# Kernel optimization log

Hardware: AMD Instinct MI355X
Metric: run time of the kernel (lower is better)

The kernel has to match this reference:

```python
import jax, jax.numpy as jnp
import numpy as np

B, N, C, H = 2, 2048, 1024, 16
D = C // H  # head_dim = 64


def setup_inputs() -> dict:
    key = jax.random.key(0)
    ks = jax.random.split(key, 5)
    s = 0.02
    return {
        "x": jax.random.normal(ks[0], (B, N, C), dtype=jnp.float32),
        "w_qkv": jax.random.normal(ks[1], (3 * C, C), dtype=jnp.float32) * s,
        "b_qkv": jnp.zeros((3 * C,), dtype=jnp.float32),
        "w_proj": jax.random.normal(ks[2], (C, C), dtype=jnp.float32) * s,
        "b_proj": jnp.zeros((C,), dtype=jnp.float32),
    }


def reference(x, w_qkv, b_qkv, w_proj, b_proj):
    scale = D ** -0.5
    # QKV projection: [B,N,3C]
    qkv = jnp.einsum('bnc,oc->bno', x, w_qkv) + b_qkv
    qkv = qkv.reshape(B, N, 3, H, D).transpose(2, 0, 3, 1, 4)  # [3,B,H,N,D]
    q, k, v = qkv[0], qkv[1], qkv[2]
    attn = jnp.einsum('bhnd,bhmd->bhnm', q, k) * scale  # [B,H,N,N]
    attn = jax.nn.softmax(attn, axis=-1)
    out = jnp.einsum('bhnm,bhmd->bhnd', attn, v)  # [B,H,N,D]
    out = out.transpose(0, 2, 1, 3).reshape(B, N, C)
    return jnp.einsum('bnc,oc->bno', out, w_proj) + b_proj
```

## Files before the change

### kernel.cpp

```cpp
#include <hip/hip_runtime.h>
#include <hip/hip_bf16.h>

typedef __attribute__((ext_vector_type(4))) float f32x4;
typedef __attribute__((ext_vector_type(16))) float f32x16;
typedef __attribute__((ext_vector_type(8))) short short8;
typedef __attribute__((ext_vector_type(4))) unsigned int u32x4;
typedef __attribute__((ext_vector_type(2))) unsigned int u32x2;
typedef unsigned short u16;

__device__ __forceinline__ u16 f2bf(float x) {
  unsigned u = __float_as_uint(x);
  u += 0x7fffu + ((u >> 16) & 1u);
  return (u16)(u >> 16);
}

__device__ __forceinline__ void gload_lds16(const void* g, void* l) {
  __builtin_amdgcn_global_load_lds(
      (__attribute__((address_space(1))) void*)g,
      (__attribute__((address_space(3))) void*)l, 16, 0, 0);
}

__global__ void cvt_all(const float* __restrict__ x, const float* __restrict__ wq,
                        const float* __restrict__ wp, ushort4* __restrict__ dst) {
  const int N1 = 1048576, N2 = 786432, NT = 2097152;
  for (int i = blockIdx.x * 256 + threadIdx.x; i < NT; i += 524288) {
    float4 v;
    if (i < N1)            v = ((const float4*)x)[i];
    else if (i < N1 + N2)  v = ((const float4*)wq)[i - N1];
    else                   v = ((const float4*)wp)[i - N1 - N2];
    ushort4 o;
    o.x = f2bf(v.x); o.y = f2bf(v.y); o.z = f2bf(v.z); o.w = f2bf(v.w);
    dst[i] = o;
  }
}

__global__ __launch_bounds__(512, 2) void gemm256_bt(
    const u16* __restrict__ A, const u16* __restrict__ B,
    const float* __restrict__ bias, u16* __restrict__ Cout,
    int M, int N, int K)
{
  __shared__ u16 LA[2][2][8192];
  __shared__ u16 LB[2][12288];

  const int tid  = threadIdx.x;
  const int w    = tid >> 6;
  const int lane = tid & 63;
  const int wm   = w >> 2;
  const int wn   = w & 3;
  const int hi   = lane >> 4;
  const int lo   = lane & 15;

  const int L  = (int)(blockIdx.x & 7) * 32 + (int)(blockIdx.x >> 3);
  const int bx = L >> 4, by = L & 15;
  const long brow = (long)by * 256;
  const long bcol = (long)bx * 192;

  f32x4 acc[8][3];
#pragma unroll
  for (int m = 0; m < 8; ++m)
#pragma unroll
    for (int n = 0; n < 3; ++n)
#pragma unroll
      for (int r = 0; r < 4; ++r) acc[m][n][r] = 0.0f;

  const int srow = lane >> 3;
  const int sg   = (lane & 7) ^ srow;
  const int l7   = lo & 7;

  auto stA = [&](int kt, int bi, int i) {
    const long k0 = (long)kt * 64;
#pragma unroll
    for (int mh = 0; mh < 2; ++mh) {
      const long r = brow + mh * 128 + i * 64 + w * 8 + srow;
      gload_lds16(A + r * K + k0 + sg * 8, &LA[bi][mh][i * 4096 + w * 512]);
    }
  };
  auto stB = [&](int kt, int bi, int u) {
    const long k0 = (long)kt * 64;
    const long r = bcol + u * 64 + w * 8 + srow;
    gload_lds16(B + r * K + k0 + sg * 8, &LB[bi][u * 4096 + w * 512]);
  };

  short8 a[4][2], b[3][2];
  auto rdA = [&](int bi, int mq) {
#pragma unroll
    for (int f = 0; f < 4; ++f) {
      const int rl = mq * 64 + f * 16 + lo;
#pragma unroll
      for (int ks = 0; ks < 2; ++ks)
        a[f][ks] = *(const short8*)(&LA[bi][wm][rl * 64 + ((ks * 4 + hi) ^ l7) * 8]);
    }
  };
  auto rdB = [&](int bi) {
#pragma unroll
    for (int f = 0; f < 3; ++f) {
      const int rl = wn * 48 + f * 16 + lo;
#pragma unroll
      for (int ks = 0; ks < 2; ++ks)
        b[f][ks] = *(const short8*)(&LB[bi][rl * 64 + ((ks * 4 + hi) ^ l7) * 8]);
    }
  };

#define MFMA24(mq)                                                                  \
  __builtin_amdgcn_s_setprio(1);                                                    \
  _Pragma("unroll")                                                                 \
  for (int f = 0; f < 4; ++f)                                                       \
    _Pragma("unroll")                                                               \
    for (int n = 0; n < 3; ++n)                                                     \
      _Pragma("unroll")                                                             \
      for (int ks = 0; ks < 2; ++ks)                                                \
        acc[(mq)*4 + f][n] = __builtin_amdgcn_mfma_f32_16x16x32_bf16(               \
            a[f][ks], b[n][ks], acc[(mq)*4 + f][n], 0, 0, 0);                       \
  __builtin_amdgcn_s_setprio(0);

#define PHASE_WAIT()                                      \
  __builtin_amdgcn_s_barrier();                           \
  asm volatile("s_waitcnt lgkmcnt(0)" ::: "memory");      \
  __builtin_amdgcn_sched_barrier(0);

  const int nkt = K >> 6;
  stA(0, 0, 0); stA(0, 0, 1); stB(0, 0, 0); stB(0, 0, 1); stB(0, 0, 2);
  stA(1, 1, 0); stA(1, 1, 1); stB(1, 1, 0); stB(1, 1, 1); stB(1, 1, 2);
  asm volatile("s_waitcnt vmcnt(7)" ::: "memory");
  __builtin_amdgcn_s_barrier();

  for (int it = 0; it < (nkt >> 1); ++it) {
    const int t2 = 2 * it + 2, t3 = 2 * it + 3;
    rdA(0, 0); rdB(0);
    if (it > 0) stA(2 * it + 1, 1, 1);
    PHASE_WAIT(); MFMA24(0); __builtin_amdgcn_s_barrier();
    rdA(0, 1);
    if (t2 < nkt) { stB(t2, 0, 0); stB(t2, 0, 1); stB(t2, 0, 2); stA(t2, 0, 0); }
    PHASE_WAIT(); MFMA24(1);
    if (t2 < nkt) { asm volatile("s_waitcnt vmcnt(5)" ::: "memory"); }
    else          { asm volatile("s_waitcnt vmcnt(0)" ::: "memory"); }
    __builtin_amdgcn_sched_barrier(0);
    __builtin_amdgcn_s_barrier();
    rdA(1, 0); rdB(1);
    if (t2 < nkt) stA(t2, 0, 1);
    PHASE_WAIT(); MFMA24(0); __builtin_amdgcn_s_barrier();
    rdA(1, 1);
    if (t3 < nkt) { stB(t3, 1, 0); stB(t3, 1, 1); stB(t3, 1, 2); stA(t3, 1, 0); }
    PHASE_WAIT(); MFMA24(1);
    if (t3 < nkt) { asm volatile("s_waitcnt vmcnt(5)" ::: "memory"); }
    __builtin_amdgcn_sched_barrier(0);
    __builtin_amdgcn_s_barrier();
  }
#undef MFMA24
#undef PHASE_WAIT

  const float SCC = 0.18033688011112042f;
  float bv[3];
#pragma unroll
  for (int n = 0; n < 3; ++n) bv[n] = bias[bcol + wn * 48 + n * 16 + lo];
#pragma unroll
  for (int m = 0; m < 8; ++m)
#pragma unroll
    for (int n = 0; n < 3; ++n) {
      const long colf = bcol + wn * 48 + n * 16;
      const float qsc = (colf < 1024) ? SCC : 1.0f;
#pragma unroll
      for (int r = 0; r < 4; ++r) {
        const long row = brow + wm * 128 + m * 16 + hi * 4 + r;
        Cout[row * (long)N + colf + lo] = f2bf((acc[m][n][r] + bv[n]) * qsc);
      }
    }
}

template<int OUT_BF16>
__global__ __launch_bounds__(256) void gemm_bt(
    const u16* __restrict__ A, const u16* __restrict__ B,
    const float* __restrict__ bias, void* __restrict__ Cout,
    int M, int N, int K)
{
  __shared__ u16 As[2][128 * 64];
  __shared__ u16 Bs[2][128 * 64];
  const int tid  = threadIdx.x;
  const int lane = tid & 63;
  const int w    = tid >> 6;
  const int wm   = w >> 1, wn = w & 1;
  const int hi   = lane >> 4;
  const int lo   = lane & 15;
  const int l7   = lo & 7;
  const long brow = (long)blockIdx.y * 128;
  const long bcol = (long)blockIdx.x * 128;

  f32x4 acc[4][4];
#pragma unroll
  for (int i = 0; i < 4; i++)
#pragma unroll
    for (int j = 0; j < 4; j++)
#pragma unroll
      for (int r = 0; r < 4; r++) acc[i][j][r] = 0.0f;

  const int srow = lane >> 3;
  const int sg   = (lane & 7) ^ srow;

  float bv[4];
#pragma unroll
  for (int fn = 0; fn < 4; fn++) bv[fn] = bias[bcol + wn * 64 + fn * 16 + lo];

  auto stage = [&](int kt, int bi) {
    const int k0 = kt << 6;
#pragma unroll
    for (int c = 0; c < 4; ++c) {
      const int chunk = (c << 2) + w;
      const int ra = (chunk << 3) + srow;
      gload_lds16(A + (size_t)(brow + ra) * K + k0 + sg * 8, &As[bi][chunk * 512]);
      gload_lds16(B + (size_t)(bcol + ra) * K + k0 + sg * 8, &Bs[bi][chunk * 512]);
    }
  };

  const int nkt = K >> 6;
  stage(0, 0);
  __syncthreads();
  int cur = 0;

  for (int kt = 0; kt < nkt; ++kt) {
    if (kt + 1 < nkt) stage(kt + 1, cur ^ 1);
#pragma unroll
    for (int ks = 0; ks < 2; ++ks) {
      short8 af[4], bfr[4];
      const int g = ((ks * 4 + hi) ^ l7) * 8;
#pragma unroll
      for (int f = 0; f < 4; f++) {
        af[f]  = *(const short8*)(&As[cur][(wm * 64 + f * 16 + lo) * 64 + g]);
        bfr[f] = *(const short8*)(&Bs[cur][(wn * 64 + f * 16 + lo) * 64 + g]);
      }
#pragma unroll
      for (int fm = 0; fm < 4; fm++)
#pragma unroll
        for (int fn = 0; fn < 4; fn++)
          acc[fm][fn] = __builtin_amdgcn_mfma_f32_16x16x32_bf16(af[fm], bfr[fn], acc[fm][fn], 0, 0, 0);
    }
    __syncthreads();
    cur ^= 1;
  }

#pragma unroll
  for (int fm = 0; fm < 4; fm++)
#pragma unroll
    for (int fn = 0; fn < 4; fn++)
#pragma unroll
      for (int r = 0; r < 4; r++) {
        const long row = brow + wm * 64 + fm * 16 + hi * 4 + r;
        const long col = bcol + wn * 64 + fn * 16 + lo;
        const float v = acc[fm][fn][r] + bv[fn];
        if (OUT_BF16) ((u16*)Cout)[row * (long)N + col] = f2bf(v);
        else          ((float*)Cout)[row * (long)N + col] = v;
      }
}

__global__ __launch_bounds__(512, 4) void attn_fused(
    const u16* __restrict__ qkv, u16* __restrict__ out)
{
  __shared__ __align__(16) char smem[65536];

  const int tid  = threadIdx.x;
  const int w    = tid >> 6;
  const int lane = tid & 63;
  const int l31  = lane & 31;
  const int hc   = lane >> 5;
  const int g1   = (lane >> 4) & 1;
  const int l15  = lane & 15;
  const int half = w >> 2;
  const int qg   = w & 3;

  const int bid  = blockIdx.x;
  const int xcd  = bid & 7;
  const int slot = bid >> 3;
  const int qb   = slot & 15;
  const int bh   = ((slot >> 4) << 3) | xcd;
  const int b    = bh >> 4, h = bh & 15;

  short8 qf[4];
  {
    const u16* qp = qkv + (size_t)(b * 2048 + qb * 128 + qg * 32 + l31) * 3072 + h * 64 + hc * 8;
#pragma unroll
    for (int ds = 0; ds < 4; ++ds) qf[ds] = *(const short8*)(qp + ds * 16);
  }

  f32x16 acc0, acc1;
#pragma unroll
  for (int r = 0; r < 16; ++r) { acc0[r] = 0.f; acc1[r] = 0.f; }
  float lsum = 0.f;

  const int srow8 = lane >> 3;
  const int kgl   = (lane & 7) ^ srow8;
  const int vkey  = (lane >> 5) * 4 + ((lane >> 1) & 3);
  const int vd    = ((lane >> 3) & 3) * 16 + (lane & 1) * 8;

  auto kbuf = [&](int bi) { return (u16*)(smem + (size_t)(half * 2 + bi) * 8192); };
  auto vbuf = [&](int bi) { return (u16*)(smem + 32768 + (size_t)(half * 2 + bi) * 8192); };

  auto stage = [&](int t, int bi) {
    const size_t rbase = (size_t)(b * 2048 + half * 1024 + t * 64);
    u16* Kb = kbuf(bi);
    u16* Vb = vbuf(bi);
#pragma unroll
    for (int c = 0; c < 2; ++c) {
      const int chunk = qg * 2 + c;
      gload_lds16(qkv + (rbase + chunk * 8 + srow8) * 3072 + 1024 + h * 64 + kgl * 8,
                  Kb + chunk * 512);
      gload_lds16(qkv + (rbase + chunk * 8 + vkey) * 3072 + 2048 + h * 64 + vd,
                  Vb + chunk * 512);
    }
  };

  stage(0, 0);
  __syncthreads();
  int cur = 0;

  for (int t = 0; t < 16; ++t) {
    if (t < 15) stage(t + 1, cur ^ 1);

    const u16* Kc = kbuf(cur);
    const unsigned va =
        (unsigned)(unsigned long long)(const __attribute__((address_space(3))) u16*)vbuf(cur);

    f32x16 s0, s1;
#pragma unroll
    for (int r = 0; r < 16; ++r) { s0[r] = 0.f; s1[r] = 0.f; }
    __builtin_amdgcn_s_setprio(1);
#pragma unroll
    for (int ds = 0; ds < 4; ++ds) {
      const int gb = (((2 * ds + hc) ^ (lane & 7)) << 4);
      const short8 k0 = *(const short8*)((const char*)Kc + l31 * 128 + gb);
      const short8 k1 = *(const short8*)((const char*)Kc + 4096 + l31 * 128 + gb);
      s0 = __builtin_amdgcn_mfma_f32_32x32x16_bf16(k0, qf[ds], s0, 0, 0, 0);
      s1 = __builtin_amdgcn_mfma_f32_32x32x16_bf16(k1, qf[ds], s1, 0, 0, 0);
    }
    __builtin_amdgcn_s_setprio(0);

    float p[32];
#pragma unroll
    for (int r = 0; r < 16; ++r) {
      p[r]      = __builtin_amdgcn_exp2f(s0[r]);
      p[16 + r] = __builtin_amdgcn_exp2f(s1[r]);
    }
    {
      float a0 = 0.f, a1 = 0.f, a2 = 0.f, a3 = 0.f;
#pragma unroll
      for (int r = 0; r < 8; ++r) {
        a0 += p[r]; a1 += p[8 + r]; a2 += p[16 + r]; a3 += p[24 + r];
      }
      lsum += (a0 + a1) + (a2 + a3);
    }

    short8 pa[4];
#pragma unroll
    for (int ks = 0; ks < 4; ++ks) {
      const int bs = ks * 8;
      unsigned X0, X1, X2, X3;
      asm("v_cvt_pk_bf16_f32 %0, %1, %2" : "=v"(X0) : "v"(p[bs + 0]), "v"(p[bs + 1]));
      asm("v_cvt_pk_bf16_f32 %0, %1, %2" : "=v"(X1) : "v"(p[bs + 2]), "v"(p[bs + 3]));
      asm("v_cvt_pk_bf16_f32 %0, %1, %2" : "=v"(X2) : "v"(p[bs + 4]), "v"(p[bs + 5]));
      asm("v_cvt_pk_bf16_f32 %0, %1, %2" : "=v"(X3) : "v"(p[bs + 6]), "v"(p[bs + 7]));
      asm("v_permlane32_swap_b32 %0, %1" : "+v"(X0), "+v"(X2));
      asm("v_permlane32_swap_b32 %0, %1" : "+v"(X1), "+v"(X3));
      u32x4 wv;
      wv[0] = X0; wv[1] = X1; wv[2] = X2; wv[3] = X3;
      pa[ks] = __builtin_bit_cast(short8, wv);
    }

#pragma unroll
    for (int dt = 0; dt < 2; ++dt) {
      const unsigned vb = va + (unsigned)(hc * 1024 + dt * 256 + g1 * 128 + l15 * 8);
      u32x2 q0, q1, q2, q3, q4, q5, q6, q7;
      asm volatile("ds_read_b64_tr_b16 %0, %1"             : "=v"(q0) : "v"(vb));
      asm volatile("ds_read_b64_tr_b16 %0, %1 offset:512"  : "=v"(q1) : "v"(vb));
      asm volatile("ds_read_b64_tr_b16 %0, %1 offset:2048" : "=v"(q2) : "v"(vb));
      asm volatile("ds_read_b64_tr_b16 %0, %1 offset:2560" : "=v"(q3) : "v"(vb));
      asm volatile("ds_read_b64_tr_b16 %0, %1 offset:4096" : "=v"(q4) : "v"(vb));
      asm volatile("ds_read_b64_tr_b16 %0, %1 offset:4608" : "=v"(q5) : "v"(vb));
      asm volatile("ds_read_b64_tr_b16 %0, %1 offset:6144" : "=v"(q6) : "v"(vb));
      asm volatile("ds_read_b64_tr_b16 %0, %1 offset:6656" : "=v"(q7) : "v"(vb));
      asm volatile("s_waitcnt lgkmcnt(0)" ::: "memory");
      __builtin_amdgcn_sched_barrier(0);
      __builtin_amdgcn_s_setprio(1);
      f32x16 A = dt ? acc1 : acc0;
      {
        u32x4 bb; bb[0] = q0[0]; bb[1] = q0[1]; bb[2] = q1[0]; bb[3] = q1[1];
        A = __builtin_amdgcn_mfma_f32_32x32x16_bf16(pa[0], __builtin_bit_cast(short8, bb), A, 0, 0, 0);
      }
      {
        u32x4 bb; bb[0] = q2[0]; bb[1] = q2[1]; bb[2] = q3[0]; bb[3] = q3[1];
        A = __builtin_amdgcn_mfma_f32_32x32x16_bf16(pa[1], __builtin_bit_cast(short8, bb), A, 0, 0, 0);
      }
      {
        u32x4 bb; bb[0] = q4[0]; bb[1] = q4[1]; bb[2] = q5[0]; bb[3] = q5[1];
        A = __builtin_amdgcn_mfma_f32_32x32x16_bf16(pa[2], __builtin_bit_cast(short8, bb), A, 0, 0, 0);
      }
      {
        u32x4 bb; bb[0] = q6[0]; bb[1] = q6[1]; bb[2] = q7[0]; bb[3] = q7[1];
        A = __builtin_amdgcn_mfma_f32_32x32x16_bf16(pa[3], __builtin_bit_cast(short8, bb), A, 0, 0, 0);
      }
      __builtin_amdgcn_s_setprio(0);
      if (dt) acc1 = A; else acc0 = A;
    }

    __syncthreads();
    cur ^= 1;
  }

  float ltot = lsum + __shfl_xor(lsum, 32);
  float* MG = (float*)smem;
  const int midx = (qg * 64 + lane) * 33;
  if (half == 1) {
#pragma unroll
    for (int r = 0; r < 16; ++r) { MG[midx + r] = acc0[r]; MG[midx + 16 + r] = acc1[r]; }
    MG[midx + 32] = ltot;
  }
  __syncthreads();
  if (half == 0) {
#pragma unroll
    for (int r = 0; r < 16; ++r) { acc0[r] += MG[midx + r]; acc1[r] += MG[midx + 16 + r]; }
    ltot += MG[midx + 32];
    const float inv = 1.0f / ltot;
    const size_t orow0 = (size_t)(b * 2048 + qb * 128 + qg * 32);
#pragma unroll
    for (int r = 0; r < 16; ++r) {
      const int rowq = (r & 3) + 8 * (r >> 2) + 4 * hc;
      const float ir = __shfl(inv, rowq);
      out[(orow0 + rowq) * 1024 + h * 64 + l31]      = f2bf(acc0[r] * ir);
      out[(orow0 + rowq) * 1024 + h * 64 + 32 + l31] = f2bf(acc1[r] * ir);
    }
  }
}

extern "C" void kernel_launch(void* const* d_in, const int* in_sizes, int n_in,
                              void* d_out, int out_size, void* d_ws, size_t ws_size,
                              hipStream_t stream) {
  const float* x      = (const float*)d_in[0];
  const float* w_qkv  = (const float*)d_in[1];
  const float* b_qkv  = (const float*)d_in[2];
  const float* w_proj = (const float*)d_in[3];
  const float* b_proj = (const float*)d_in[4];
  float* out = (float*)d_out;

  char* ws = (char*)d_ws;
  u16* xb     = (u16*)(ws);
  u16* wqkvb  = (u16*)(ws + (8ull  << 20));
  u16* wprojb = (u16*)(ws + (14ull << 20));
  u16* qkvb   = (u16*)(ws + (16ull << 20));
  u16* aob    = (u16*)(ws + (40ull << 20));

  cvt_all<<<2048, 256, 0, stream>>>(x, w_qkv, w_proj, (ushort4*)ws);

  gemm256_bt<<<256, 512, 0, stream>>>(xb, wqkvb, b_qkv, qkvb, 4096, 3072, 1024);

  attn_fused<<<512, 512, 0, stream>>>(qkvb, aob);

  gemm_bt<0><<<dim3(8, 32), 256, 0, stream>>>(aob, wprojb, b_proj, out, 4096, 1024, 1024);
}
```

Before: 107.0 us.

## Split attention KV range across three wave groups with single-buffered V

Raises the attention block from two to three 4-wave groups. Each group processes an 11- or 10-tile slice of the 32 KV tiles instead of 16, and the groups' partial outputs and row sums are merged through shared memory at the end. K stays double-buffered, but V now has a single buffer per group and is staged after a mid-iteration barrier, with explicit vmcnt waits and raw s_barrier replacing __syncthreads. The aim is a shorter serial loop per wave and more parallelism per block. The cost is extra barriers per tile, less overlap on V loads, one group idling on its last iteration, and more LDS and threads per block, which may lower occupancy.

Measured after the change: 350.7 us. 228% more time.

```diff
diff --git a/kernel.cpp b/kernel.cpp
--- a/kernel.cpp
+++ b/kernel.cpp
@@ -251,10 +251,10 @@
       }
 }
 
-__global__ __launch_bounds__(512, 4) void attn_fused(
+__global__ __launch_bounds__(768, 6) void attn_fused(
     const u16* __restrict__ qkv, u16* __restrict__ out)
 {
-  __shared__ __align__(16) char smem[65536];
+  __shared__ __align__(16) char smem[73728];
 
   const int tid  = threadIdx.x;
   const int w    = tid >> 6;
@@ -263,7 +263,7 @@
   const int hc   = lane >> 5;
   const int g1   = (lane >> 4) & 1;
   const int l15  = lane & 15;
-  const int half = w >> 2;
+  const int third = w >> 2;
   const int qg   = w & 3;
 
   const int bid  = blockIdx.x;
@@ -273,6 +273,9 @@
   const int bh   = ((slot >> 4) << 3) | xcd;
   const int b    = bh >> 4, h = bh & 15;
 
+  const int ntiles = (third < 2) ? 11 : 10;
+  const int st     = third * 11;
+
   short8 qf[4];
   {
     const u16* qp = qkv + (size_t)(b * 2048 + qb * 128 + qg * 32 + l31) * 3072 + h * 64 + hc * 8;
@@ -290,132 +293,161 @@
   const int vkey  = (lane >> 5) * 4 + ((lane >> 1) & 3);
   const int vd    = ((lane >> 3) & 3) * 16 + (lane & 1) * 8;
 
-  auto kbuf = [&](int bi) { return (u16*)(smem + (size_t)(half * 2 + bi) * 8192); };
-  auto vbuf = [&](int bi) { return (u16*)(smem + 32768 + (size_t)(half * 2 + bi) * 8192); };
-
-  auto stage = [&](int t, int bi) {
-    const size_t rbase = (size_t)(b * 2048 + half * 1024 + t * 64);
+  auto kbuf = [&](int bi) { return (u16*)(smem + (size_t)(third * 2 + bi) * 8192); };
+  u16* vb = (u16*)(smem + 49152 + (size_t)third * 8192);
+
+  auto stK = [&](int t, int bi) {
+    const size_t rbase = (size_t)(b * 2048 + t * 64);
     u16* Kb = kbuf(bi);
-    u16* Vb = vbuf(bi);
 #pragma unroll
     for (int c = 0; c < 2; ++c) {
       const int chunk = qg * 2 + c;
       gload_lds16(qkv + (rbase + chunk * 8 + srow8) * 3072 + 1024 + h * 64 + kgl * 8,
                   Kb + chunk * 512);
+    }
+  };
+  auto stV = [&](int t) {
+    const size_t rbase = (size_t)(b * 2048 + t * 64);
+#pragma unroll
+    for (int c = 0; c < 2; ++c) {
+      const int chunk = qg * 2 + c;
       gload_lds16(qkv + (rbase + chunk * 8 + vkey) * 3072 + 2048 + h * 64 + vd,
-                  Vb + chunk * 512);
-    }
-  };
-
-  stage(0, 0);
-  __syncthreads();
+                  vb + chunk * 512);
+    }
+  };
+
+  stK(st, 0); stV(st);
+  asm volatile("s_waitcnt vmcnt(0)" ::: "memory");
+  __builtin_amdgcn_s_barrier();
   int cur = 0;
 
-  for (int t = 0; t < 16; ++t) {
-    if (t < 15) stage(t + 1, cur ^ 1);
-
-    const u16* Kc = kbuf(cur);
-    const unsigned va =
-        (unsigned)(unsigned long long)(const __attribute__((address_space(3))) u16*)vbuf(cur);
+  for (int tt = 0; tt < 11; ++tt) {
+    const bool act = tt < ntiles;
+    const bool pfK = (tt + 1) < ntiles;
+    const int  t   = st + tt;
+
+    if (pfK) stK(t + 1, cur ^ 1);
 
     f32x16 s0, s1;
 #pragma unroll
     for (int r = 0; r < 16; ++r) { s0[r] = 0.f; s1[r] = 0.f; }
-    __builtin_amdgcn_s_setprio(1);
-#pragma unroll
-    for (int ds = 0; ds < 4; ++ds) {
-      const int gb = (((2 * ds + hc) ^ (lane & 7)) << 4);
-      const short8 k0 = *(const short8*)((const char*)Kc + l31 * 128 + gb);
-      const short8 k1 = *(const short8*)((const char*)Kc + 4096 + l31 * 128 + gb);
-      s0 = __builtin_amdgcn_mfma_f32_32x32x16_bf16(k0, qf[ds], s0, 0, 0, 0);
-      s1 = __builtin_amdgcn_mfma_f32_32x32x16_bf16(k1, qf[ds], s1, 0, 0, 0);
-    }
-    __builtin_amdgcn_s_setprio(0);
-
-    float p[32];
-#pragma unroll
-    for (int r = 0; r < 16; ++r) {
-      p[r]      = __builtin_amdgcn_exp2f(s0[r]);
-      p[16 + r] = __builtin_amdgcn_exp2f(s1[r]);
-    }
-    {
-      float a0 = 0.f, a1 = 0.f, a2 = 0.f, a3 = 0.f;
-#pragma unroll
-      for (int r = 0; r < 8; ++r) {
-        a0 += p[r]; a1 += p[8 + r]; a2 += p[16 + r]; a3 += p[24 + r];
-      }
-      lsum += (a0 + a1) + (a2 + a3);
-    }
-
     short8 pa[4];
-#pragma unroll
-    for (int ks = 0; ks < 4; ++ks) {
-      const int bs = ks * 8;
-      unsigned X0, X1, X2, X3;
-      asm("v_cvt_pk_bf16_f32 %0, %1, %2" : "=v"(X0) : "v"(p[bs + 0]), "v"(p[bs + 1]));
-      asm("v_cvt_pk_bf16_f32 %0, %1, %2" : "=v"(X1) : "v"(p[bs + 2]), "v"(p[bs + 3]));
-      asm("v_cvt_pk_bf16_f32 %0, %1, %2" : "=v"(X2) : "v"(p[bs + 4]), "v"(p[bs + 5]));
-      asm("v_cvt_pk_bf16_f32 %0, %1, %2" : "=v"(X3) : "v"(p[bs + 6]), "v"(p[bs + 7]));
-      asm("v_permlane32_swap_b32 %0, %1" : "+v"(X0), "+v"(X2));
-      asm("v_permlane32_swap_b32 %0, %1" : "+v"(X1), "+v"(X3));
-      u32x4 wv;
-      wv[0] = X0; wv[1] = X1; wv[2] = X2; wv[3] = X3;
-      pa[ks] = __builtin_bit_cast(short8, wv);
-    }
-
-#pragma unroll
-    for (int dt = 0; dt < 2; ++dt) {
-      const unsigned vb = va + (unsigned)(hc * 1024 + dt * 256 + g1 * 128 + l15 * 8);
-      u32x2 q0, q1, q2, q3, q4, q5, q6, q7;
-      asm volatile("ds_read_b64_tr_b16 %0, %1"             : "=v"(q0) : "v"(vb));
-      asm volatile("ds_read_b64_tr_b16 %0, %1 offset:512"  : "=v"(q1) : "v"(vb));
-      asm volatile("ds_read_b64_tr_b16 %0, %1 offset:2048" : "=v"(q2) : "v"(vb));
-      asm volatile("ds_read_b64_tr_b16 %0, %1 offset:2560" : "=v"(q3) : "v"(vb));
-      asm volatile("ds_read_b64_tr_b16 %0, %1 offset:4096" : "=v"(q4) : "v"(vb));
-      asm volatile("ds_read_b64_tr_b16 %0, %1 offset:4608" : "=v"(q5) : "v"(vb));
-      asm volatile("ds_read_b64_tr_b16 %0, %1 offset:6144" : "=v"(q6) : "v"(vb));
-      asm volatile("ds_read_b64_tr_b16 %0, %1 offset:6656" : "=v"(q7) : "v"(vb));
-      asm volatile("s_waitcnt lgkmcnt(0)" ::: "memory");
-      __builtin_amdgcn_sched_barrier(0);
+
+    if (act) {
+      const u16* Kc = kbuf(cur);
       __builtin_amdgcn_s_setprio(1);
-      f32x16 A = dt ? acc1 : acc0;
+#pragma unroll
+      for (int ds = 0; ds < 4; ++ds) {
+        const int gb = (((2 * ds + hc) ^ (lane & 7)) << 4);
+        const short8 k0 = *(const short8*)((const char*)Kc + l31 * 128 + gb);
+        const short8 k1 = *(const short8*)((const char*)Kc + 4096 + l31 * 128 + gb);
+        s0 = __builtin_amdgcn_mfma_f32_32x32x16_bf16(k0, qf[ds], s0, 0, 0, 0);
+        s1 = __builtin_amdgcn_mfma_f32_32x32x16_bf16(k1, qf[ds], s1, 0, 0, 0);
+      }
+      __builtin_amdgcn_s_setprio(0);
+
+      float p[32];
+#pragma unroll
+      for (int r = 0; r < 16; ++r) {
+        p[r]      = __builtin_amdgcn_exp2f(s0[r]);
+        p[16 + r] = __builtin_amdgcn_exp2f(s1[r]);
+      }
       {
-        u32x4 bb; bb[0] = q0[0]; bb[1] = q0[1]; bb[2] = q1[0]; bb[3] = q1[1];
-        A = __builtin_amdgcn_mfma_f32_32x32x16_bf16(pa[0], __builtin_bit_cast(short8, bb), A, 0, 0, 0);
-      }
-      {
-        u32x4 bb; bb[0] = q2[0]; bb[1] = q2[1]; bb[2] = q3[0]; bb[3] = q3[1];
-        A = __builtin_amdgcn_mfma_f32_32x32x16_bf16(pa[1], __builtin_bit_cast(short8, bb), A, 0, 0, 0);
-      }
-      {
-        u32x4 bb; bb[0] = q4[0]; bb[1] = q4[1]; bb[2] = q5[0]; bb[3] = q5[1];
-        A = __builtin_amdgcn_mfma_f32_32x32x16_bf16(pa[2], __builtin_bit_cast(short8, bb), A, 0, 0, 0);
-      }
-      {
-        u32x4 bb; bb[0] = q6[0]; bb[1] = q6[1]; bb[2] = q7[0]; bb[3] = q7[1];
-        A = __builtin_amdgcn_mfma_f32_32x32x16_bf16(pa[3], __builtin_bit_cast(short8, bb), A, 0, 0, 0);
-      }
-      __builtin_amdgcn_s_setprio(0);
-      if (dt) acc1 = A; else acc0 = A;
-    }
-
-    __syncthreads();
+        float a0 = 0.f, a1 = 0.f, a2 = 0.f, a3 = 0.f;
+#pragma unroll
+        for (int r = 0; r < 8; ++r) {
+          a0 += p[r]; a1 += p[8 + r]; a2 += p[16 + r]; a3 += p[24 + r];
+        }
+        lsum += (a0 + a1) + (a2 + a3);
+      }
+
+#pragma unroll
+      for (int ks = 0; ks < 4; ++ks) {
+        const int bs = ks * 8;
+        unsigned X0, X1, X2, X3;
+        asm("v_cvt_pk_bf16_f32 %0, %1, %2" : "=v"(X0) : "v"(p[bs + 0]), "v"(p[bs + 1]));
+        asm("v_cvt_pk_bf16_f32 %0, %1, %2" : "=v"(X1) : "v"(p[bs + 2]), "v"(p[bs + 3]));
+        asm("v_cvt_pk_bf16_f32 %0, %1, %2" : "=v"(X2) : "v"(p[bs + 4]), "v"(p[bs + 5]));
+        asm("v_cvt_pk_bf16_f32 %0, %1, %2" : "=v"(X3) : "v"(p[bs + 6]), "v"(p[bs + 7]));
+        asm("v_permlane32_swap_b32 %0, %1" : "+v"(X0), "+v"(X2));
+        asm("v_permlane32_swap_b32 %0, %1" : "+v"(X1), "+v"(X3));
+        u32x4 wv;
+        wv[0] = X0; wv[1] = X1; wv[2] = X2; wv[3] = X3;
+        pa[ks] = __builtin_bit_cast(short8, wv);
+      }
+    }
+
+    if (pfK) { asm volatile("s_waitcnt vmcnt(2)" ::: "memory"); }
+    else     { asm volatile("s_waitcnt vmcnt(0)" ::: "memory"); }
+    __builtin_amdgcn_sched_barrier(0);
+    __builtin_amdgcn_s_barrier();
+
+    if (act) {
+      const unsigned va =
+          (unsigned)(unsigned long long)(const __attribute__((address_space(3))) u16*)vb;
+#pragma unroll
+      for (int dt = 0; dt < 2; ++dt) {
+        const unsigned vba = va + (unsigned)(hc * 1024 + dt * 256 + g1 * 128 + l15 * 8);
+        u32x2 q0, q1, q2, q3, q4, q5, q6, q7;
+        asm volatile("ds_read_b64_tr_b16 %0, %1"             : "=v"(q0) : "v"(vba));
+        asm volatile("ds_read_b64_tr_b16 %0, %1 offset:512"  : "=v"(q1) : "v"(vba));
+        asm volatile("ds_read_b64_tr_b16 %0, %1 offset:2048" : "=v"(q2) : "v"(vba));
+        asm volatile("ds_read_b64_tr_b16 %0, %1 offset:2560" : "=v"(q3) : "v"(vba));
+        asm volatile("ds_read_b64_tr_b16 %0, %1 offset:4096" : "=v"(q4) : "v"(vba));
+        asm volatile("ds_read_b64_tr_b16 %0, %1 offset:4608" : "=v"(q5) : "v"(vba));
+        asm volatile("ds_read_b64_tr_b16 %0, %1 offset:6144" : "=v"(q6) : "v"(vba));
+        asm volatile("ds_read_b64_tr_b16 %0, %1 offset:6656" : "=v"(q7) : "v"(vba));
+        asm volatile("s_waitcnt lgkmcnt(0)" ::: "memory");
+        __builtin_amdgcn_sched_barrier(0);
+        __builtin_amdgcn_s_setprio(1);
+        f32x16 A = dt ? acc1 : acc0;
+        {
+          u32x4 bb; bb[0] = q0[0]; bb[1] = q0[1]; bb[2] = q1[0]; bb[3] = q1[1];
+          A = __builtin_amdgcn_mfma_f32_32x32x16_bf16(pa[0], __builtin_bit_cast(short8, bb), A, 0, 0, 0);
+        }
+        {
+          u32x4 bb; bb[0] = q2[0]; bb[1] = q2[1]; bb[2] = q3[0]; bb[3] = q3[1];
+          A = __builtin_amdgcn_mfma_f32_32x32x16_bf16(pa[1], __builtin_bit_cast(short8, bb), A, 0, 0, 0);
+        }
+        {
+          u32x4 bb; bb[0] = q4[0]; bb[1] = q4[1]; bb[2] = q5[0]; bb[3] = q5[1];
+          A = __builtin_amdgcn_mfma_f32_32x32x16_bf16(pa[2], __builtin_bit_cast(short8, bb), A, 0, 0, 0);
+        }
+        {
+          u32x4 bb; bb[0] = q6[0]; bb[1] = q6[1]; bb[2] = q7[0]; bb[3] = q7[1];
+          A = __builtin_amdgcn_mfma_f32_32x32x16_bf16(pa[3], __builtin_bit_cast(short8, bb), A, 0, 0, 0);
+        }
+        __builtin_amdgcn_s_setprio(0);
+        if (dt) acc1 = A; else acc0 = A;
+      }
+    }
+
+    asm volatile("s_waitcnt vmcnt(0)" ::: "memory");
+    __builtin_amdgcn_sched_barrier(0);
+    __builtin_amdgcn_s_barrier();
+
+    if (pfK) stV(t + 1);
     cur ^= 1;
   }
 
   float ltot = lsum + __shfl_xor(lsum, 32);
   float* MG = (float*)smem;
-  const int midx = (qg * 64 + lane) * 33;
-  if (half == 1) {
+  if (third > 0) {
+    const int midx = ((third - 1) * 256 + qg * 64 + lane) * 33;
 #pragma unroll
     for (int r = 0; r < 16; ++r) { MG[midx + r] = acc0[r]; MG[midx + 16 + r] = acc1[r]; }
     MG[midx + 32] = ltot;
   }
   __syncthreads();
-  if (half == 0) {
-#pragma unroll
-    for (int r = 0; r < 16; ++r) { acc0[r] += MG[midx + r]; acc1[r] += MG[midx + 16 + r]; }
-    ltot += MG[midx + 32];
+  if (third == 0) {
+    const int m0 = (qg * 64 + lane) * 33;
+    const int m1 = (256 + qg * 64 + lane) * 33;
+#pragma unroll
+    for (int r = 0; r < 16; ++r) {
+      acc0[r] += MG[m0 + r] + MG[m1 + r];
+      acc1[r] += MG[m0 + 16 + r] + MG[m1 + 16 + r];
+    }
+    ltot += MG[m0 + 32] + MG[m1 + 32];
     const float inv = 1.0f / ltot;
     const size_t orow0 = (size_t)(b * 2048 + qb * 128 + qg * 32);
 #pragma unroll
@@ -449,7 +481,7 @@
 
   gemm256_bt<<<256, 512, 0, stream>>>(xb, wqkvb, b_qkv, qkvb, 4096, 3072, 1024);
 
-  attn_fused<<<512, 512, 0, stream>>>(qkvb, aob);
+  attn_fused<<<512, 768, 0, stream>>>(qkvb, aob);
 
   gemm_bt<0><<<dim3(8, 32), 256, 0, stream>>>(aob, wprojb, b_proj, out, 4096, 1024, 1024);
 }
```
